# Kernel tuning notes

Measured on AMD Instinct MI355X. Metric: run time of the kernel, lower is better.

The kernel has to match this reference:

```python
import jax, jax.numpy as jnp
import numpy as np

N, D, MAX_DEG, B = 100000, 256, 128, 1024
FANOUTS = (25, 10)
OUT = 128  # per-branch output dim; concat doubles it


def setup_inputs() -> dict:
    key = jax.random.key(0)
    ks = jax.random.split(key, 8)
    s1 = 1.0 / np.sqrt(D)
    return {
        "ids": jax.random.randint(ks[0], (B,), 0, N),
        "adj": jax.random.randint(ks[1], (N, MAX_DEG), 0, N),
        "feats": jax.random.normal(ks[2], (N, D), dtype=jnp.float32),
        "W1x": jax.random.normal(ks[3], (OUT, D), dtype=jnp.float32) * s1,
        "b1x": jnp.zeros((OUT,), jnp.float32),
        "W1n": jax.random.normal(ks[4], (OUT, D), dtype=jnp.float32) * s1,
        "b1n": jnp.zeros((OUT,), jnp.float32),
        "W2x": jax.random.normal(ks[5], (OUT, 2 * OUT), dtype=jnp.float32) * s1,
        "b2x": jnp.zeros((OUT,), jnp.float32),
        "W2n": jax.random.normal(ks[6], (OUT, 2 * OUT), dtype=jnp.float32) * s1,
        "b2n": jnp.zeros((OUT,), jnp.float32),
    }


def _sample(adj, ids, n_samples, key):
    # uniform_neib_sampler: one shared random column permutation, take first n
    perm = jax.random.permutation(key, adj.shape[1])
    return adj[ids][:, perm[:n_samples]].reshape(-1)  # flattened neighbor ids


def _agg(x, neibs, Wx, bx, Wn, bn, act):
    # MeanAggregator: concat(fc_x(x), fc_neib(mean over neighbors))
    m = neibs.reshape(x.shape[0], -1, neibs.shape[-1]).mean(axis=1)
    out = jnp.concatenate([x @ Wx.T + bx, m @ Wn.T + bn], axis=-1)
    return act(out) if act is not None else out


def reference(ids, adj, feats, W1x, b1x, W1n, b1n, W2x, b2x, W2n, b2n):
    k1, k2 = jax.random.split(jax.random.key(42))
    ids1 = _sample(adj, ids, FANOUTS[0], k1)      # [B*25]
    ids2 = _sample(adj, ids1, FANOUTS[1], k2)     # [B*25*10]
    h = [feats[ids], feats[ids1], feats[ids2]]    # gathers: the memory-bound core
    # layer 1 (relu) applied to each consecutive (self, neighbor) pair
    h = [_agg(h[k], h[k + 1], W1x, b1x, W1n, b1n, jax.nn.relu) for k in range(2)]
    # layer 2 (no activation)
    h = [_agg(h[0], h[1], W2x, b2x, W2n, b2n, None)]
    return h[0]  # [B, 256]
```

## Files before the change

### kernel.cpp

```cpp
#include <hip/hip_runtime.h>
#include <stdint.h>
#include <stddef.h>
#include <algorithm>


#define D       256
#define D4      64
#define BATCH   1024
#define F1      25
#define F2      10
#define MAXDEG  128
#define OUTD    128
#define SP      264
#define ZP      260

struct Perms { int p1[F1]; int p2[F2]; };

static inline uint32_t rotl32(uint32_t x, int d){ return (x<<d)|(x>>(32-d)); }

static void tf2x32(uint32_t k0, uint32_t k1, uint32_t x0, uint32_t x1,
                   uint32_t* o0, uint32_t* o1){
  uint32_t ks0=k0, ks1=k1, ks2 = k0^k1^0x1BD11BDAu;
  static const int rot[2][4] = {{13,15,26,6},{17,29,16,24}};
  x0 += ks0; x1 += ks1;
  for (int g=0; g<5; ++g){
    const int* r = rot[g&1];
    for (int i=0;i<4;++i){ x0 += x1; x1 = rotl32(x1, r[i]) ^ x0; }
    switch(g){
      case 0: x0 += ks1; x1 += ks2 + 1u; break;
      case 1: x0 += ks2; x1 += ks0 + 2u; break;
      case 2: x0 += ks0; x1 += ks1 + 3u; break;
      case 3: x0 += ks1; x1 += ks2 + 4u; break;
      default:x0 += ks2; x1 += ks0 + 5u; break;
    }
  }
  *o0 = x0; *o1 = x1;
}

static void mkperm(uint32_t ka, uint32_t kb, int n, int* outp){
  uint32_t ska, skb;
  tf2x32(ka, kb, 0u, 1u, &ska, &skb);
  uint32_t bits[MAXDEG];
  int idxs[MAXDEG];
  for (int i=0;i<MAXDEG;++i){
    uint32_t y0,y1; tf2x32(ska,skb, 0u,(uint32_t)i, &y0,&y1);
    bits[i] = y0 ^ y1;
    idxs[i] = i;
  }
  std::stable_sort(idxs, idxs+MAXDEG,
                   [&](int a,int b){ return bits[a] < bits[b]; });
  for (int j=0;j<n;++j) outp[j] = idxs[j];
}

static void compute_perms(Perms& P){
  uint32_t k1a,k1b,k2a,k2b;
  tf2x32(0u,42u, 0u,0u, &k1a,&k1b);
  tf2x32(0u,42u, 0u,1u, &k2a,&k2b);
  mkperm(k1a,k1b, F1, P.p1);
  mkperm(k2a,k2b, F2, P.p2);
}

typedef short s16x8 __attribute__((ext_vector_type(8)));
typedef float f32x4 __attribute__((ext_vector_type(4)));

__device__ __forceinline__ uint16_t f2bf(float f){
  uint32_t u = __float_as_uint(f);
  u += 0x7fffu + ((u >> 16) & 1u);
  return (uint16_t)(u >> 16);
}
__device__ __forceinline__ float bf2f(uint16_t h){
  return __uint_as_float(((uint32_t)h) << 16);
}

__global__ __launch_bounds__(256) void pack_k(
    const float* __restrict__ W1x, const float* __restrict__ W1n,
    const float* __restrict__ W2x, const float* __restrict__ W2n,
    uint16_t* __restrict__ WB, float* __restrict__ W2T){
  int g = blockIdx.x*256 + threadIdx.x;
  if (g < 8192){
    int kt = g >> 10, ct = (g >> 6) & 15, lane = g & 63;
    int n = ct*16 + (lane & 15);
    int k = kt*32 + (lane >> 4)*8;
    const float* src = (n < OUTD) ? (W1x + (size_t)n*D + k)
                                  : (W1n + (size_t)(n-OUTD)*D + k);
    float4 f0 = *(const float4*)src;
    float4 f1 = *(const float4*)(src + 4);
    uint32_t p[4] = {
      (uint32_t)f2bf(f0.x) | ((uint32_t)f2bf(f0.y)<<16),
      (uint32_t)f2bf(f0.z) | ((uint32_t)f2bf(f0.w)<<16),
      (uint32_t)f2bf(f1.x) | ((uint32_t)f2bf(f1.y)<<16),
      (uint32_t)f2bf(f1.z) | ((uint32_t)f2bf(f1.w)<<16) };
    *(uint4*)(WB + (size_t)g*8) = *(uint4*)p;
  } else {
    int idx = g - 8192;
    int k = idx >> 8, o = idx & 255;
    W2T[idx] = (o < OUTD) ? W2x[(size_t)o*D + k]
                          : W2n[(size_t)(o-OUTD)*D + k];
  }
}

__global__ __launch_bounds__(256) void mean_k(
    const float4* __restrict__ feats4,
    const int* __restrict__ ids, const int* __restrict__ adj,
    uint16_t* __restrict__ M1b, Perms P)
{
  const int lane = threadIdx.x & 63;
  const int r = blockIdx.x*4 + (threadIdx.x >> 6);
  const int b = r / F1, j = r - b*F1;
  const int id = ids[b];
  const int i1 = adj[(size_t)id*MAXDEG + P.p1[j]];
  int nid[F2];
  #pragma unroll
  for (int u=0;u<F2;++u) nid[u] = adj[(size_t)i1*MAXDEG + P.p2[u]];
  float4 s = {0.f,0.f,0.f,0.f};
  #pragma unroll
  for (int u=0;u<F2;++u){
    float4 v = feats4[(size_t)nid[u]*D4 + lane];
    s.x+=v.x; s.y+=v.y; s.z+=v.z; s.w+=v.w;
  }
  const float inv = 1.f/F2;
  uint32_t p[2] = { (uint32_t)f2bf(s.x*inv) | ((uint32_t)f2bf(s.y*inv)<<16),
                    (uint32_t)f2bf(s.z*inv) | ((uint32_t)f2bf(s.w*inv)<<16) };
  *(uint2*)(M1b + (size_t)r*D + lane*4) = *(uint2*)p;
}

__global__ __launch_bounds__(256, 4) void mega5_k(
    const float4* __restrict__ feats4,
    const int* __restrict__ ids, const int* __restrict__ adj,
    const uint16_t* __restrict__ M1b, const uint16_t* __restrict__ WB,
    const float* __restrict__ W2T,
    const float* __restrict__ b1x, const float* __restrict__ b1n,
    const float* __restrict__ b2x, const float* __restrict__ b2n,
    float* __restrict__ out, Perms P)
{
  __shared__ uint16_t S[64*SP];
  __shared__ float    M2s[D];
  __shared__ float    Z0s[D];
  __shared__ int      sids[26];
  uint16_t* Z = S;

  const int b    = blockIdx.x;
  const int tid  = threadIdx.x;
  const int lane = tid & 63;
  const int w    = tid >> 6;
  const int ln   = lane & 15;
  const int q    = lane >> 4;
  const int id   = ids[b];

  if (tid < F1) sids[tid] = adj[(size_t)id*MAXDEG + P.p1[tid]];
  if (tid == F1) sids[F1] = id;
  __syncthreads();

  float4 va[7];
  uint2  vm[7];
  #pragma unroll
  for (int l=0;l<7;++l){
    int idx = tid + l*256;
    if (idx < 26*D4)
      va[l] = feats4[(size_t)sids[idx>>6]*D4 + (idx&63)];
  }
  #pragma unroll
  for (int l=0;l<7;++l){
    int idx = tid + l*256;
    if (idx < F1*D4)
      vm[l] = *(const uint2*)(M1b + (size_t)(b*F1 + (idx>>6))*D + (idx&63)*4);
  }
  #pragma unroll
  for (int l=0;l<7;++l){
    int idx = tid + l*256;
    if (idx < 26*D4){
      int r = idx>>6, c4 = idx&63;
      uint32_t p[2] = { (uint32_t)f2bf(va[l].x) | ((uint32_t)f2bf(va[l].y)<<16),
                        (uint32_t)f2bf(va[l].z) | ((uint32_t)f2bf(va[l].w)<<16) };
      *(uint2*)(S + r*SP + c4*4) = *(uint2*)p;
    }
  }
  #pragma unroll
  for (int l=0;l<7;++l){
    int idx = tid + l*256;
    if (idx < F1*D4){
      int r = idx>>6, c4 = idx&63;
      *(uint2*)(S + (26+r)*SP + c4*4) = vm[l];
    }
  }
  __syncthreads();

  {
    float s = 0.f;
    #pragma unroll
    for (int r=0;r<F1;++r) s += bf2f(S[r*SP + tid]);
    S[51*SP + tid] = f2bf(s * (1.f/F1));
  }
  __syncthreads();

  f32x4 acc[4][4];
  #pragma unroll
  for (int mt=0;mt<4;++mt)
    #pragma unroll
    for (int nt=0;nt<4;++nt) acc[mt][nt] = (f32x4){0.f,0.f,0.f,0.f};

  #pragma unroll 2
  for (int kt = 0; kt < 8; ++kt){
    s16x8 af[4], bf[4];
    #pragma unroll
    for (int mt=0;mt<4;++mt)
      af[mt] = *(const s16x8*)(S + (mt*16 + ln)*SP + kt*32 + q*8);
    #pragma unroll
    for (int nt=0;nt<4;++nt)
      bf[nt] = *(const s16x8*)(WB + (size_t)((kt*16 + w*4 + nt)*64 + lane)*8);
    #pragma unroll
    for (int mt=0;mt<4;++mt)
      #pragma unroll
      for (int nt=0;nt<4;++nt)
        acc[mt][nt] = __builtin_amdgcn_mfma_f32_16x16x32_bf16(
                        af[mt], bf[nt], acc[mt][nt], 0, 0, 0);
  }
  __syncthreads();

  {
    const bool left = (w < 2);
    float bia[4];
    #pragma unroll
    for (int nt=0;nt<4;++nt){
      int n = w*64 + nt*16 + ln;
      bia[nt] = left ? b1x[n] : b1n[n-OUTD];
    }
    #pragma unroll
    for (int mt=0;mt<4;++mt)
      #pragma unroll
      for (int nt=0;nt<4;++nt){
        int n = w*64 + nt*16 + ln;
        #pragma unroll
        for (int reg=0;reg<4;++reg){
          int m = mt*16 + q*4 + reg;
          float val = fmaxf(acc[mt][nt][reg] + bia[nt], 0.f);
          if (left){
            if (m < 26) Z[m*ZP + n] = f2bf(val);
            if (m == 25) Z0s[n] = val;
          } else {
            if (m >= 26 && m < 52) Z[(m-26)*ZP + n] = f2bf(val);
            if (m == 51) Z0s[n] = val;
          }
        }
      }
  }
  __syncthreads();

  {
    float s = 0.f;
    #pragma unroll
    for (int r=0;r<F1;++r) s += bf2f(Z[r*ZP + tid]);
    M2s[tid] = s * (1.f/F1);
  }
  __syncthreads();

  {
    const int o = tid;
    const float* zsrc = (o < OUTD) ? Z0s : M2s;
    float acc2 = 0.f;
    #pragma unroll 4
    for (int k4=0;k4<D4;++k4){
      float4 z = *(const float4*)(zsrc + k4*4);
      acc2 += z.x * W2T[(size_t)(k4*4+0)*D + o];
      acc2 += z.y * W2T[(size_t)(k4*4+1)*D + o];
      acc2 += z.z * W2T[(size_t)(k4*4+2)*D + o];
      acc2 += z.w * W2T[(size_t)(k4*4+3)*D + o];
    }
    acc2 += (o < OUTD) ? b2x[o] : b2n[o-OUTD];
    out[(size_t)b*D + o] = acc2;
  }
}

extern "C" void kernel_launch(void* const* d_in, const int* in_sizes, int n_in,
                              void* d_out, int out_size, void* d_ws, size_t ws_size,
                              hipStream_t stream){
  const int*   ids   = (const int*)  d_in[0];
  const int*   adj   = (const int*)  d_in[1];
  const float* feats = (const float*)d_in[2];
  const float* W1x   = (const float*)d_in[3];
  const float* b1x   = (const float*)d_in[4];
  const float* W1n   = (const float*)d_in[5];
  const float* b1n   = (const float*)d_in[6];
  const float* W2x   = (const float*)d_in[7];
  const float* b2x   = (const float*)d_in[8];
  const float* W2n   = (const float*)d_in[9];
  const float* b2n   = (const float*)d_in[10];
  float* out = (float*)d_out;

  Perms P;
  compute_perms(P);

  char* wsb = (char*)d_ws;
  uint16_t* M1b = (uint16_t*)wsb;
  wsb += (size_t)BATCH*F1*D*sizeof(uint16_t);
  uint16_t* WB  = (uint16_t*)wsb;
  wsb += (size_t)8192*8*sizeof(uint16_t);
  float*    W2T = (float*)wsb;

  hipLaunchKernelGGL(pack_k, dim3(288), dim3(256), 0, stream,
                     W1x, W1n, W2x, W2n, WB, W2T);
  hipLaunchKernelGGL(mean_k, dim3(BATCH*F1/4), dim3(256), 0, stream,
                     (const float4*)feats, ids, adj, M1b, P);
  hipLaunchKernelGGL(mega5_k, dim3(BATCH), dim3(256), 0, stream,
                     (const float4*)feats, ids, adj, M1b, WB, W2T,
                     b1x, b1n, b2x, b2n, out, P);
}
```

Baseline: 233.7 us.

## Fuse second-hop neighbor mean into main kernel, removing intermediate buffer

The separate mean_k kernel that gathered second-hop neighbors and wrote bf16 means to a global workspace is removed. Each block of the main kernel now resolves its own 250 neighbor indices into shared memory and computes the 25 means directly into the shared tile. This removes the global write and read-back of the intermediate means and one kernel launch. The trade-off is fewer independent blocks issuing the dominant random gathers, with each wave looping serially over its neighbor rows, which may expose more memory latency.

```diff
diff --git a/kernel.cpp b/kernel.cpp
--- a/kernel.cpp
+++ b/kernel.cpp
@@ -99,36 +99,10 @@
   }
 }
 
-__global__ __launch_bounds__(256) void mean_k(
+__global__ __launch_bounds__(256, 4) void mega6_k(
     const float4* __restrict__ feats4,
     const int* __restrict__ ids, const int* __restrict__ adj,
-    uint16_t* __restrict__ M1b, Perms P)
-{
-  const int lane = threadIdx.x & 63;
-  const int r = blockIdx.x*4 + (threadIdx.x >> 6);
-  const int b = r / F1, j = r - b*F1;
-  const int id = ids[b];
-  const int i1 = adj[(size_t)id*MAXDEG + P.p1[j]];
-  int nid[F2];
-  #pragma unroll
-  for (int u=0;u<F2;++u) nid[u] = adj[(size_t)i1*MAXDEG + P.p2[u]];
-  float4 s = {0.f,0.f,0.f,0.f};
-  #pragma unroll
-  for (int u=0;u<F2;++u){
-    float4 v = feats4[(size_t)nid[u]*D4 + lane];
-    s.x+=v.x; s.y+=v.y; s.z+=v.z; s.w+=v.w;
-  }
-  const float inv = 1.f/F2;
-  uint32_t p[2] = { (uint32_t)f2bf(s.x*inv) | ((uint32_t)f2bf(s.y*inv)<<16),
-                    (uint32_t)f2bf(s.z*inv) | ((uint32_t)f2bf(s.w*inv)<<16) };
-  *(uint2*)(M1b + (size_t)r*D + lane*4) = *(uint2*)p;
-}
-
-__global__ __launch_bounds__(256, 4) void mega5_k(
-    const float4* __restrict__ feats4,
-    const int* __restrict__ ids, const int* __restrict__ adj,
-    const uint16_t* __restrict__ M1b, const uint16_t* __restrict__ WB,
-    const float* __restrict__ W2T,
+    const uint16_t* __restrict__ WB, const float* __restrict__ W2T,
     const float* __restrict__ b1x, const float* __restrict__ b1n,
     const float* __restrict__ b2x, const float* __restrict__ b2n,
     float* __restrict__ out, Perms P)
@@ -137,7 +111,7 @@
   __shared__ float    M2s[D];
   __shared__ float    Z0s[D];
   __shared__ int      sids[26];
-  uint16_t* Z = S;
+  __shared__ int      nidx[F1*F2];
 
   const int b    = blockIdx.x;
   const int tid  = threadIdx.x;
@@ -146,24 +120,41 @@
   const int ln   = lane & 15;
   const int q    = lane >> 4;
   const int id   = ids[b];
+  uint16_t* Z = S;
 
   if (tid < F1) sids[tid] = adj[(size_t)id*MAXDEG + P.p1[tid]];
   if (tid == F1) sids[F1] = id;
   __syncthreads();
+  if (tid < F1*F2){
+    int j = tid / F2, u = tid - (tid/F2)*F2;
+    nidx[tid] = adj[(size_t)sids[j]*MAXDEG + P.p2[u]];
+  }
+  __syncthreads();
 
   float4 va[7];
-  uint2  vm[7];
   #pragma unroll
   for (int l=0;l<7;++l){
     int idx = tid + l*256;
     if (idx < 26*D4)
       va[l] = feats4[(size_t)sids[idx>>6]*D4 + (idx&63)];
   }
-  #pragma unroll
-  for (int l=0;l<7;++l){
-    int idx = tid + l*256;
-    if (idx < F1*D4)
-      vm[l] = *(const uint2*)(M1b + (size_t)(b*F1 + (idx>>6))*D + (idx&63)*4);
+  #pragma unroll 2
+  for (int t=0;t<7;++t){
+    int j = w + 4*t;
+    if (j < F1){
+      const int* np = &nidx[j*F2];
+      float4 s = {0.f,0.f,0.f,0.f};
+      #pragma unroll
+      for (int u=0;u<F2;++u){
+        float4 v = feats4[(size_t)np[u]*D4 + lane];
+        s.x+=v.x; s.y+=v.y; s.z+=v.z; s.w+=v.w;
+      }
+      const float inv = 1.f/F2;
+      uint32_t p[2] = {
+        (uint32_t)f2bf(s.x*inv) | ((uint32_t)f2bf(s.y*inv)<<16),
+        (uint32_t)f2bf(s.z*inv) | ((uint32_t)f2bf(s.w*inv)<<16) };
+      *(uint2*)(S + (26+j)*SP + lane*4) = *(uint2*)p;
+    }
   }
   #pragma unroll
   for (int l=0;l<7;++l){
@@ -173,14 +164,6 @@
       uint32_t p[2] = { (uint32_t)f2bf(va[l].x) | ((uint32_t)f2bf(va[l].y)<<16),
                         (uint32_t)f2bf(va[l].z) | ((uint32_t)f2bf(va[l].w)<<16) };
       *(uint2*)(S + r*SP + c4*4) = *(uint2*)p;
-    }
-  }
-  #pragma unroll
-  for (int l=0;l<7;++l){
-    int idx = tid + l*256;
-    if (idx < F1*D4){
-      int r = idx>>6, c4 = idx&63;
-      *(uint2*)(S + (26+r)*SP + c4*4) = vm[l];
     }
   }
   __syncthreads();
@@ -291,17 +274,13 @@
   compute_perms(P);
 
   char* wsb = (char*)d_ws;
-  uint16_t* M1b = (uint16_t*)wsb;
-  wsb += (size_t)BATCH*F1*D*sizeof(uint16_t);
   uint16_t* WB  = (uint16_t*)wsb;
   wsb += (size_t)8192*8*sizeof(uint16_t);
   float*    W2T = (float*)wsb;
 
   hipLaunchKernelGGL(pack_k, dim3(288), dim3(256), 0, stream,
                      W1x, W1n, W2x, W2n, WB, W2T);
-  hipLaunchKernelGGL(mean_k, dim3(BATCH*F1/4), dim3(256), 0, stream,
-                     (const float4*)feats, ids, adj, M1b, P);
-  hipLaunchKernelGGL(mega5_k, dim3(BATCH), dim3(256), 0, stream,
-                     (const float4*)feats, ids, adj, M1b, WB, W2T,
+  hipLaunchKernelGGL(mega6_k, dim3(BATCH), dim3(256), 0, stream,
+                     (const float4*)feats, ids, adj, WB, W2T,
                      b1x, b1n, b2x, b2n, out, P);
 }
```

New measurement: 225.7 us. 3.4% less time.
